# Kernel optimization log

Measured on AMD Instinct MI355X. Metric: run time of the kernel, lower is better.

The kernel has to match this reference:

```python
import jax, jax.numpy as jnp
import numpy as np

N_NODES = 100000
D_IN = 256
D_OUT = 128
N_EDGES = 1600000


def setup_inputs() -> dict:
    key = jax.random.key(0)
    k1, k2, k3, k4 = jax.random.split(key, 4)
    x = jax.random.normal(k1, (N_NODES, D_IN), dtype=jnp.float32)
    edge_index = jax.random.randint(k2, (2, N_EDGES), 0, N_NODES, dtype=jnp.int64)
    # GCNConv parameters (glorot-style scale)
    W = jax.random.normal(k3, (D_IN, D_OUT), dtype=jnp.float32) * (1.0 / np.sqrt(D_IN))
    b = jax.random.normal(k4, (D_OUT,), dtype=jnp.float32) * 0.01
    return {"x": x, "edge_index": edge_index, "W": W, "b": b}


def reference(x, edge_index, W, b):
    n = x.shape[0]
    # add self-loops (PyG GCNConv default)
    loop = jnp.arange(n, dtype=edge_index.dtype)
    src = jnp.concatenate([edge_index[0], loop])
    dst = jnp.concatenate([edge_index[1], loop])
    # symmetric normalization: deg^-1/2[src] * deg^-1/2[dst]
    ones = jnp.ones(src.shape[0], dtype=x.dtype)
    deg = jax.ops.segment_sum(ones, dst, num_segments=n)
    dinv = jnp.where(deg > 0, jax.lax.rsqrt(deg), 0.0)
    norm = dinv[src] * dinv[dst]  # [E+N]
    # linear transform at nodes, then gather-scale-scatter over edges
    h = x @ W  # [N, d_out]
    msg = h[src] * norm[:, None]  # [E+N, d_out]
    out = jax.ops.segment_sum(msg, dst, num_segments=n) + b
    # CRD.forward: relu then dropout (identity in eval mode)
    return jax.nn.relu(out)
```

## Files before the change

kernel.cpp:

```cpp
#include <hip/hip_runtime.h>
#include <stdint.h>

#define D_IN 256
#define D_OUT 128
#define MAXB 800
#define NCHUNK 256

typedef __attribute__((ext_vector_type(8))) short bf16x8;
typedef __attribute__((ext_vector_type(4))) float f32x4;

__device__ __forceinline__ unsigned short f2bf(float f) {
  union { float f; uint32_t u; } v; v.f = f;
  uint32_t u = v.u;
  uint32_t r = (u + 0x7FFFu + ((u >> 16) & 1u)) >> 16;
  return (unsigned short)r;
}
__device__ __forceinline__ float bf_lo(uint32_t u) {
  union { uint32_t u; float f; } v; v.u = u << 16; return v.f;
}
__device__ __forceinline__ float bf_hi(uint32_t u) {
  union { uint32_t u; float f; } v; v.u = u & 0xFFFF0000u; return v.f;
}

__global__ __launch_bounds__(256) void k_conv_w(const float* __restrict__ W,
                                                unsigned short* __restrict__ wt) {
  int idx = blockIdx.x * 256 + threadIdx.x;
  int n = idx >> 8;
  int k = idx & 255;
  wt[idx] = f2bf(W[k * D_OUT + n]);
}

__global__ __launch_bounds__(256) void k_gemm(const float* __restrict__ x,
                                              const unsigned short* __restrict__ wt,
                                              unsigned short* __restrict__ hp, int N) {
  int wave = threadIdx.x >> 6;
  int lane = threadIdx.x & 63;
  int m = lane & 15;
  int q = lane >> 4;
  int r0 = blockIdx.x * 64 + wave * 16;
  if (r0 >= N) return;

  bf16x8 a[8];
  const float* xrow = x + (size_t)(r0 + m) * D_IN + q * 8;
#pragma unroll
  for (int kt = 0; kt < 8; ++kt) {
    float4 u0 = *reinterpret_cast<const float4*>(xrow + kt * 32);
    float4 u1 = *reinterpret_cast<const float4*>(xrow + kt * 32 + 4);
    bf16x8 av;
    av[0] = (short)f2bf(u0.x); av[1] = (short)f2bf(u0.y);
    av[2] = (short)f2bf(u0.z); av[3] = (short)f2bf(u0.w);
    av[4] = (short)f2bf(u1.x); av[5] = (short)f2bf(u1.y);
    av[6] = (short)f2bf(u1.z); av[7] = (short)f2bf(u1.w);
    a[kt] = av;
  }

#pragma unroll
  for (int nt = 0; nt < 8; ++nt) {
    f32x4 acc = {0.f, 0.f, 0.f, 0.f};
    const unsigned short* wrow = wt + (size_t)(nt * 16 + m) * D_IN + q * 8;
#pragma unroll
    for (int kt = 0; kt < 8; ++kt) {
      bf16x8 bv = *reinterpret_cast<const bf16x8*>(wrow + kt * 32);
      acc = __builtin_amdgcn_mfma_f32_16x16x32_bf16(a[kt], bv, acc, 0, 0, 0);
    }
#pragma unroll
    for (int r = 0; r < 4; ++r) {
      int row = r0 + q * 4 + r;
      hp[(size_t)row * D_OUT + nt * 16 + m] = f2bf(acc[r]);
    }
  }
}

__global__ __launch_bounds__(256) void k_passA(const int* __restrict__ ei, int E, int CH,
                                               int NB, int* __restrict__ cntm) {
  __shared__ int bins[MAXB];
  int c = blockIdx.x;
  for (int b = threadIdx.x; b < NB; b += 256) bins[b] = 0;
  __syncthreads();
  int start = c * CH, end = min(E, start + CH);
  for (int eb = start + (int)threadIdx.x * 4; eb < end; eb += 1024) {
    int kmax = end - eb; if (kmax > 4) kmax = 4;
    if (kmax == 4) {
      int4 v = *reinterpret_cast<const int4*>(ei + E + eb);
      atomicAdd(&bins[v.x >> 7], 1);
      atomicAdd(&bins[v.y >> 7], 1);
      atomicAdd(&bins[v.z >> 7], 1);
      atomicAdd(&bins[v.w >> 7], 1);
    } else {
      for (int k = 0; k < kmax; ++k) atomicAdd(&bins[ei[E + eb + k] >> 7], 1);
    }
  }
  __syncthreads();
  for (int b = threadIdx.x; b < NB; b += 256) cntm[(size_t)b * NCHUNK + c] = bins[b];
}

__global__ __launch_bounds__(NCHUNK) void k_scanB1(const int* __restrict__ cntm,
                                                   int* __restrict__ ofs,
                                                   int* __restrict__ tot) {
  __shared__ int sc[NCHUNK];
  int b = blockIdx.x, t = threadIdx.x;
  int v = cntm[(size_t)b * NCHUNK + t];
  sc[t] = v;
  __syncthreads();
  for (int off = 1; off < NCHUNK; off <<= 1) {
    int val = (t >= off) ? sc[t - off] : 0;
    __syncthreads();
    sc[t] += val;
    __syncthreads();
  }
  ofs[(size_t)b * NCHUNK + t] = sc[t] - v;
  if (t == NCHUNK - 1) tot[b] = sc[t];
}

__global__ __launch_bounds__(256) void k_scanB2(const int* __restrict__ tot,
                                                int* __restrict__ base, int NB,
                                                int* __restrict__ nptr, int N, int E) {
  __shared__ int sc[256];
  int t = threadIdx.x;
  int v[4];
  int s = 0;
#pragma unroll
  for (int j = 0; j < 4; ++j) {
    int i = t * 4 + j;
    v[j] = (i < NB) ? tot[i] : 0;
    s += v[j];
  }
  sc[t] = s;
  __syncthreads();
  for (int off = 1; off < 256; off <<= 1) {
    int val = (t >= off) ? sc[t - off] : 0;
    __syncthreads();
    sc[t] += val;
    __syncthreads();
  }
  int ex = sc[t] - s;
#pragma unroll
  for (int j = 0; j < 4; ++j) {
    int i = t * 4 + j;
    if (i < NB) base[i] = ex;
    ex += v[j];
  }
  if (t == 0) nptr[N] = E;
}

__global__ __launch_bounds__(256) void k_passC(const int* __restrict__ ei, int E, int CH,
                                               int NB, const int* __restrict__ ofs,
                                               const int* __restrict__ base,
                                               int* __restrict__ P) {
  __shared__ int cur[MAXB];
  int c = blockIdx.x;
  for (int b = threadIdx.x; b < NB; b += 256)
    cur[b] = base[b] + ofs[(size_t)b * NCHUNK + c];
  __syncthreads();
  int start = c * CH, end = min(E, start + CH);
  for (int eb = start + (int)threadIdx.x * 4; eb < end; eb += 1024) {
    int kmax = end - eb; if (kmax > 4) kmax = 4;
    int s4[4], d4[4];
    if (kmax == 4) {
      int4 vs = *reinterpret_cast<const int4*>(ei + eb);
      int4 vd = *reinterpret_cast<const int4*>(ei + E + eb);
      s4[0] = vs.x; s4[1] = vs.y; s4[2] = vs.z; s4[3] = vs.w;
      d4[0] = vd.x; d4[1] = vd.y; d4[2] = vd.z; d4[3] = vd.w;
    } else {
      for (int k = 0; k < kmax; ++k) { s4[k] = ei[eb + k]; d4[k] = ei[E + eb + k]; }
    }
#pragma unroll
    for (int k = 0; k < 4; ++k) {
      if (k >= kmax) break;
      int d = d4[k];
      int p = atomicAdd(&cur[d >> 7], 1);
      P[p] = s4[k] | ((d & 127) << 17);
    }
  }
}

__global__ __launch_bounds__(256) void k_sortd(const int* __restrict__ P,
                                               const int* __restrict__ base,
                                               const int* __restrict__ tot,
                                               int* __restrict__ nptr,
                                               float* __restrict__ dinv,
                                               int* __restrict__ P2, int N) {
  __shared__ int ideg[128];
  __shared__ int sc[128];
  __shared__ int cur[128];
  int b = blockIdx.x, t = threadIdx.x;
  if (t < 128) ideg[t] = 0;
  __syncthreads();
  int s0 = base[b], T = tot[b];
  for (int i = s0 + t; i < s0 + T; i += 256) atomicAdd(&ideg[P[i] >> 17], 1);
  __syncthreads();
  if (t < 128) sc[t] = ideg[t];
  __syncthreads();
  for (int off = 1; off < 128; off <<= 1) {
    int v = (t < 128 && t >= off) ? sc[t - off] : 0;
    __syncthreads();
    if (t < 128) sc[t] += v;
    __syncthreads();
  }
  if (t < 128) {
    int exc = s0 + sc[t] - ideg[t];
    int node = b * 128 + t;
    if (node < N) {
      nptr[node] = exc;
      dinv[node] = rsqrtf(1.0f + (float)ideg[t]);
    }
    cur[t] = exc;
  }
  __syncthreads();
  for (int i = s0 + t; i < s0 + T; i += 256) {
    int pk = P[i];
    int p = atomicAdd(&cur[pk >> 17], 1);
    P2[p] = pk & 0x1FFFF;
  }
}

__global__ __launch_bounds__(256) void k_agg(const int* __restrict__ P2,
                                             const int* __restrict__ nptr,
                                             const uint4* __restrict__ hrows,
                                             const float* __restrict__ dinv,
                                             const float* __restrict__ bias,
                                             float* __restrict__ out, int N) {
  int wave = threadIdx.x >> 6, lane = threadIdx.x & 63;
  int node = blockIdx.x * 4 + wave;
  if (node >= N) return;
  int rs = nptr[node], re = nptr[node + 1];
  int j = lane >> 4, c = lane & 15;

  float acc[8];
#pragma unroll
  for (int k = 0; k < 8; ++k) acc[k] = 0.f;

  for (int e = rs + j; e < re; e += 4) {
    int src = P2[e];
    float r = dinv[src];
    uint4 u = hrows[(size_t)src * 16 + c];
    acc[0] += r * bf_lo(u.x); acc[1] += r * bf_hi(u.x);
    acc[2] += r * bf_lo(u.y); acc[3] += r * bf_hi(u.y);
    acc[4] += r * bf_lo(u.z); acc[5] += r * bf_hi(u.z);
    acc[6] += r * bf_lo(u.w); acc[7] += r * bf_hi(u.w);
  }
#pragma unroll
  for (int k = 0; k < 8; ++k) {
    acc[k] += __shfl_xor(acc[k], 16);
    acc[k] += __shfl_xor(acc[k], 32);
  }
  if (j == 0) {
    float rsn = dinv[node];
    uint4 uh = hrows[(size_t)node * 16 + c];
    float self[8] = {bf_lo(uh.x), bf_hi(uh.x), bf_lo(uh.y), bf_hi(uh.y),
                     bf_lo(uh.z), bf_hi(uh.z), bf_lo(uh.w), bf_hi(uh.w)};
    const float4* b4 = reinterpret_cast<const float4*>(bias);
    float4 b0 = b4[c * 2], b1 = b4[c * 2 + 1];
    float bb[8] = {b0.x, b0.y, b0.z, b0.w, b1.x, b1.y, b1.z, b1.w};
    float o[8];
#pragma unroll
    for (int k = 0; k < 8; ++k) {
      float v = rsn * (acc[k] + rsn * self[k]) + bb[k];
      o[k] = v > 0.f ? v : 0.f;
    }
    float4* orow = reinterpret_cast<float4*>(out + (size_t)node * D_OUT + c * 8);
    orow[0] = float4{o[0], o[1], o[2], o[3]};
    orow[1] = float4{o[4], o[5], o[6], o[7]};
  }
}

extern "C" void kernel_launch(void* const* d_in, const int* in_sizes, int n_in,
                              void* d_out, int out_size, void* d_ws, size_t ws_size,
                              hipStream_t stream) {
  const float* x = (const float*)d_in[0];
  const int* ei = (const int*)d_in[1];
  const float* W = (const float*)d_in[2];
  const float* bias = (const float*)d_in[3];
  int N = in_sizes[0] / D_IN;
  int E = in_sizes[1] / 2;
  float* out = (float*)d_out;

  int NB = (N + 127) >> 7;
  int CH = ((E + NCHUNK - 1) / NCHUNK + 3) & ~3;

  char* w = (char*)d_ws;
  size_t off = 0;
  auto alloc = [&](size_t bytes) -> void* {
    void* p = w + off;
    off = (off + bytes + 255) & ~(size_t)255;
    return p;
  };
  unsigned short* wt = (unsigned short*)alloc((size_t)D_IN * D_OUT * 2);
  unsigned short* hp = (unsigned short*)alloc((size_t)N * D_OUT * 2);
  float* dinv = (float*)alloc((size_t)N * 4);
  int* cntm = (int*)alloc((size_t)NB * NCHUNK * 4);
  int* ofs = (int*)alloc((size_t)NB * NCHUNK * 4);
  int* tot = (int*)alloc((size_t)NB * 4);
  int* base = (int*)alloc((size_t)NB * 4);
  int* nptr = (int*)alloc((size_t)(N + 1) * 4);
  int* P = (int*)alloc((size_t)E * 4);
  int* P2 = (int*)alloc((size_t)E * 4);
  (void)ws_size; (void)n_in; (void)out_size;

  k_conv_w<<<(D_IN * D_OUT) / 256, 256, 0, stream>>>(W, wt);
  k_gemm<<<(N + 63) / 64, 256, 0, stream>>>(x, wt, hp, N);
  k_passA<<<NCHUNK, 256, 0, stream>>>(ei, E, CH, NB, cntm);
  k_scanB1<<<NB, NCHUNK, 0, stream>>>(cntm, ofs, tot);
  k_scanB2<<<1, 256, 0, stream>>>(tot, base, NB, nptr, N, E);
  k_passC<<<NCHUNK, 256, 0, stream>>>(ei, E, CH, NB, ofs, base, P);
  k_sortd<<<NB, 256, 0, stream>>>(P, base, tot, nptr, dinv, P2, N);
  k_agg<<<(N + 3) / 4, 256, 0, stream>>>(P2, nptr, (const uint4*)hp, dinv, bias, out, N);
}
```

Measured before the change: 327.4 us.

## Co-schedule GEMM blocks with CSR build kernels and merge small launches

Merges the weight conversion into the histogram kernel and folds the second-level scan into the placement kernel, so each block recomputes the bin bases. The node GEMM is split across two grids, running alongside the placement and per-bin sort kernels so its dense work overlaps their atomic-bound phases. The GEMM loop is reordered to stream x with a one-step prefetch, keeping eight accumulators live instead of eight A fragments. The aggregation loop is unrolled by two for more loads in flight. Risks are redundant scan work in every placement block, higher register pressure, and a fixed 3:5 GEMM split that may not match the relative cost of the two stages.

```diff
diff --git a/kernel.cpp b/kernel.cpp
--- a/kernel.cpp
+++ b/kernel.cpp
@@ -22,59 +22,60 @@
   union { uint32_t u; float f; } v; v.u = u & 0xFFFF0000u; return v.f;
 }
 
-__global__ __launch_bounds__(256) void k_conv_w(const float* __restrict__ W,
-                                                unsigned short* __restrict__ wt) {
-  int idx = blockIdx.x * 256 + threadIdx.x;
-  int n = idx >> 8;
-  int k = idx & 255;
-  wt[idx] = f2bf(W[k * D_OUT + n]);
-}
-
-__global__ __launch_bounds__(256) void k_gemm(const float* __restrict__ x,
-                                              const unsigned short* __restrict__ wt,
-                                              unsigned short* __restrict__ hp, int N) {
-  int wave = threadIdx.x >> 6;
-  int lane = threadIdx.x & 63;
-  int m = lane & 15;
-  int q = lane >> 4;
-  int r0 = blockIdx.x * 64 + wave * 16;
+__device__ __forceinline__ void gemm_block(int bid, const float* __restrict__ x,
+                                           const unsigned short* __restrict__ wt,
+                                           unsigned short* __restrict__ hp, int N) {
+  int wave = threadIdx.x >> 6, lane = threadIdx.x & 63;
+  int m = lane & 15, q = lane >> 4;
+  int r0 = bid * 64 + wave * 16;
   if (r0 >= N) return;
-
-  bf16x8 a[8];
   const float* xrow = x + (size_t)(r0 + m) * D_IN + q * 8;
+
+  f32x4 acc[8];
+#pragma unroll
+  for (int nt = 0; nt < 8; ++nt) acc[nt] = f32x4{0.f, 0.f, 0.f, 0.f};
+
+  float4 u0 = *reinterpret_cast<const float4*>(xrow);
+  float4 u1 = *reinterpret_cast<const float4*>(xrow + 4);
 #pragma unroll
   for (int kt = 0; kt < 8; ++kt) {
-    float4 u0 = *reinterpret_cast<const float4*>(xrow + kt * 32);
-    float4 u1 = *reinterpret_cast<const float4*>(xrow + kt * 32 + 4);
-    bf16x8 av;
-    av[0] = (short)f2bf(u0.x); av[1] = (short)f2bf(u0.y);
-    av[2] = (short)f2bf(u0.z); av[3] = (short)f2bf(u0.w);
-    av[4] = (short)f2bf(u1.x); av[5] = (short)f2bf(u1.y);
-    av[6] = (short)f2bf(u1.z); av[7] = (short)f2bf(u1.w);
-    a[kt] = av;
-  }
-
-#pragma unroll
-  for (int nt = 0; nt < 8; ++nt) {
-    f32x4 acc = {0.f, 0.f, 0.f, 0.f};
-    const unsigned short* wrow = wt + (size_t)(nt * 16 + m) * D_IN + q * 8;
-#pragma unroll
-    for (int kt = 0; kt < 8; ++kt) {
-      bf16x8 bv = *reinterpret_cast<const bf16x8*>(wrow + kt * 32);
-      acc = __builtin_amdgcn_mfma_f32_16x16x32_bf16(a[kt], bv, acc, 0, 0, 0);
-    }
-#pragma unroll
-    for (int r = 0; r < 4; ++r) {
-      int row = r0 + q * 4 + r;
-      hp[(size_t)row * D_OUT + nt * 16 + m] = f2bf(acc[r]);
-    }
-  }
-}
-
-__global__ __launch_bounds__(256) void k_passA(const int* __restrict__ ei, int E, int CH,
-                                               int NB, int* __restrict__ cntm) {
+    float4 n0, n1;
+    if (kt < 7) {
+      n0 = *reinterpret_cast<const float4*>(xrow + (kt + 1) * 32);
+      n1 = *reinterpret_cast<const float4*>(xrow + (kt + 1) * 32 + 4);
+    }
+    bf16x8 a;
+    a[0] = (short)f2bf(u0.x); a[1] = (short)f2bf(u0.y);
+    a[2] = (short)f2bf(u0.z); a[3] = (short)f2bf(u0.w);
+    a[4] = (short)f2bf(u1.x); a[5] = (short)f2bf(u1.y);
+    a[6] = (short)f2bf(u1.z); a[7] = (short)f2bf(u1.w);
+    const unsigned short* wbase = wt + q * 8 + kt * 32;
+#pragma unroll
+    for (int nt = 0; nt < 8; ++nt) {
+      bf16x8 bv = *reinterpret_cast<const bf16x8*>(wbase + (size_t)(nt * 16 + m) * D_IN);
+      acc[nt] = __builtin_amdgcn_mfma_f32_16x16x32_bf16(a, bv, acc[nt], 0, 0, 0);
+    }
+    u0 = n0; u1 = n1;
+  }
+#pragma unroll
+  for (int nt = 0; nt < 8; ++nt)
+#pragma unroll
+    for (int r = 0; r < 4; ++r)
+      hp[(size_t)(r0 + q * 4 + r) * D_OUT + nt * 16 + m] = f2bf(acc[nt][r]);
+}
+
+__global__ __launch_bounds__(256) void k_prep(const float* __restrict__ W,
+                                              unsigned short* __restrict__ wt,
+                                              const int* __restrict__ ei, int E, int CH,
+                                              int NB, int* __restrict__ cntm) {
   __shared__ int bins[MAXB];
-  int c = blockIdx.x;
+  if (blockIdx.x < 128) {
+    int idx = blockIdx.x * 256 + threadIdx.x;
+    int n = idx >> 8, k = idx & 255;
+    wt[idx] = f2bf(W[k * D_OUT + n]);
+    return;
+  }
+  int c = blockIdx.x - 128;
   for (int b = threadIdx.x; b < NB; b += 256) bins[b] = 0;
   __syncthreads();
   int start = c * CH, end = min(E, start + CH);
@@ -94,9 +95,9 @@
   for (int b = threadIdx.x; b < NB; b += 256) cntm[(size_t)b * NCHUNK + c] = bins[b];
 }
 
-__global__ __launch_bounds__(NCHUNK) void k_scanB1(const int* __restrict__ cntm,
-                                                   int* __restrict__ ofs,
-                                                   int* __restrict__ tot) {
+__global__ __launch_bounds__(NCHUNK) void k_scan1(const int* __restrict__ cntm,
+                                                  int* __restrict__ ofs,
+                                                  int* __restrict__ tot) {
   __shared__ int sc[NCHUNK];
   int b = blockIdx.x, t = threadIdx.x;
   int v = cntm[(size_t)b * NCHUNK + t];
@@ -112,13 +113,20 @@
   if (t == NCHUNK - 1) tot[b] = sc[t];
 }
 
-__global__ __launch_bounds__(256) void k_scanB2(const int* __restrict__ tot,
-                                                int* __restrict__ base, int NB,
-                                                int* __restrict__ nptr, int N, int E) {
+__global__ __launch_bounds__(256, 4) void k_place_gemm(
+    const int* __restrict__ ei, int E, int CH, int NB,
+    const int* __restrict__ ofs, const int* __restrict__ tot,
+    int* __restrict__ basep, int* __restrict__ P,
+    const float* __restrict__ x, const unsigned short* __restrict__ wt,
+    unsigned short* __restrict__ hp, int N) {
   __shared__ int sc[256];
-  int t = threadIdx.x;
-  int v[4];
-  int s = 0;
+  __shared__ int cur[MAXB];
+  if (blockIdx.x >= NCHUNK) {
+    gemm_block(blockIdx.x - NCHUNK, x, wt, hp, N);
+    return;
+  }
+  int c = blockIdx.x, t = threadIdx.x;
+  int v[4]; int s = 0;
 #pragma unroll
   for (int j = 0; j < 4; ++j) {
     int i = t * 4 + j;
@@ -137,23 +145,15 @@
 #pragma unroll
   for (int j = 0; j < 4; ++j) {
     int i = t * 4 + j;
-    if (i < NB) base[i] = ex;
+    if (i < NB) cur[i] = ex + ofs[(size_t)i * NCHUNK + c];
     ex += v[j];
   }
-  if (t == 0) nptr[N] = E;
-}
-
-__global__ __launch_bounds__(256) void k_passC(const int* __restrict__ ei, int E, int CH,
-                                               int NB, const int* __restrict__ ofs,
-                                               const int* __restrict__ base,
-                                               int* __restrict__ P) {
-  __shared__ int cur[MAXB];
-  int c = blockIdx.x;
-  for (int b = threadIdx.x; b < NB; b += 256)
-    cur[b] = base[b] + ofs[(size_t)b * NCHUNK + c];
-  __syncthreads();
+  __syncthreads();
+  if (c == 0) {
+    for (int b = t; b < NB; b += 256) basep[b] = cur[b];
+  }
   int start = c * CH, end = min(E, start + CH);
-  for (int eb = start + (int)threadIdx.x * 4; eb < end; eb += 1024) {
+  for (int eb = start + t * 4; eb < end; eb += 1024) {
     int kmax = end - eb; if (kmax > 4) kmax = 4;
     int s4[4], d4[4];
     if (kmax == 4) {
@@ -174,19 +174,24 @@
   }
 }
 
-__global__ __launch_bounds__(256) void k_sortd(const int* __restrict__ P,
-                                               const int* __restrict__ base,
-                                               const int* __restrict__ tot,
-                                               int* __restrict__ nptr,
-                                               float* __restrict__ dinv,
-                                               int* __restrict__ P2, int N) {
+__global__ __launch_bounds__(256, 4) void k_sort_gemm(
+    const int* __restrict__ P, const int* __restrict__ basep,
+    const int* __restrict__ tot, int* __restrict__ nptr, float* __restrict__ dinv,
+    int* __restrict__ P2, int N, int E, int NB,
+    const float* __restrict__ x, const unsigned short* __restrict__ wt,
+    unsigned short* __restrict__ hp, int Goff) {
   __shared__ int ideg[128];
   __shared__ int sc[128];
   __shared__ int cur[128];
+  if (blockIdx.x >= (unsigned)NB) {
+    gemm_block(blockIdx.x - NB + Goff, x, wt, hp, N);
+    return;
+  }
   int b = blockIdx.x, t = threadIdx.x;
+  if (b == 0 && t == 0) nptr[N] = E;
   if (t < 128) ideg[t] = 0;
   __syncthreads();
-  int s0 = base[b], T = tot[b];
+  int s0 = basep[b], T = tot[b];
   for (int i = s0 + t; i < s0 + T; i += 256) atomicAdd(&ideg[P[i] >> 17], 1);
   __syncthreads();
   if (t < 128) sc[t] = ideg[t];
@@ -230,14 +235,29 @@
 #pragma unroll
   for (int k = 0; k < 8; ++k) acc[k] = 0.f;
 
-  for (int e = rs + j; e < re; e += 4) {
-    int src = P2[e];
-    float r = dinv[src];
-    uint4 u = hrows[(size_t)src * 16 + c];
-    acc[0] += r * bf_lo(u.x); acc[1] += r * bf_hi(u.x);
-    acc[2] += r * bf_lo(u.y); acc[3] += r * bf_hi(u.y);
-    acc[4] += r * bf_lo(u.z); acc[5] += r * bf_hi(u.z);
-    acc[6] += r * bf_lo(u.w); acc[7] += r * bf_hi(u.w);
+  int e = rs + j;
+  for (; e + 4 < re; e += 8) {
+    int sA = P2[e], sB = P2[e + 4];
+    float rA = dinv[sA], rB = dinv[sB];
+    uint4 uA = hrows[(size_t)sA * 16 + c];
+    uint4 uB = hrows[(size_t)sB * 16 + c];
+    acc[0] += rA * bf_lo(uA.x) + rB * bf_lo(uB.x);
+    acc[1] += rA * bf_hi(uA.x) + rB * bf_hi(uB.x);
+    acc[2] += rA * bf_lo(uA.y) + rB * bf_lo(uB.y);
+    acc[3] += rA * bf_hi(uA.y) + rB * bf_hi(uB.y);
+    acc[4] += rA * bf_lo(uA.z) + rB * bf_lo(uB.z);
+    acc[5] += rA * bf_hi(uA.z) + rB * bf_hi(uB.z);
+    acc[6] += rA * bf_lo(uA.w) + rB * bf_lo(uB.w);
+    acc[7] += rA * bf_hi(uA.w) + rB * bf_hi(uB.w);
+  }
+  if (e < re) {
+    int sA = P2[e];
+    float rA = dinv[sA];
+    uint4 uA = hrows[(size_t)sA * 16 + c];
+    acc[0] += rA * bf_lo(uA.x); acc[1] += rA * bf_hi(uA.x);
+    acc[2] += rA * bf_lo(uA.y); acc[3] += rA * bf_hi(uA.y);
+    acc[4] += rA * bf_lo(uA.z); acc[5] += rA * bf_hi(uA.z);
+    acc[6] += rA * bf_lo(uA.w); acc[7] += rA * bf_hi(uA.w);
   }
 #pragma unroll
   for (int k = 0; k < 8; ++k) {
@@ -291,18 +311,21 @@
   int* cntm = (int*)alloc((size_t)NB * NCHUNK * 4);
   int* ofs = (int*)alloc((size_t)NB * NCHUNK * 4);
   int* tot = (int*)alloc((size_t)NB * 4);
-  int* base = (int*)alloc((size_t)NB * 4);
+  int* basep = (int*)alloc((size_t)NB * 4);
   int* nptr = (int*)alloc((size_t)(N + 1) * 4);
   int* P = (int*)alloc((size_t)E * 4);
   int* P2 = (int*)alloc((size_t)E * 4);
   (void)ws_size; (void)n_in; (void)out_size;
 
-  k_conv_w<<<(D_IN * D_OUT) / 256, 256, 0, stream>>>(W, wt);
-  k_gemm<<<(N + 63) / 64, 256, 0, stream>>>(x, wt, hp, N);
-  k_passA<<<NCHUNK, 256, 0, stream>>>(ei, E, CH, NB, cntm);
-  k_scanB1<<<NB, NCHUNK, 0, stream>>>(cntm, ofs, tot);
-  k_scanB2<<<1, 256, 0, stream>>>(tot, base, NB, nptr, N, E);
-  k_passC<<<NCHUNK, 256, 0, stream>>>(ei, E, CH, NB, ofs, base, P);
-  k_sortd<<<NB, 256, 0, stream>>>(P, base, tot, nptr, dinv, P2, N);
+  int Gg = (N + 63) / 64;
+  int Gg1 = (Gg * 3) / 5;
+  int Gg2 = Gg - Gg1;
+
+  k_prep<<<128 + NCHUNK, 256, 0, stream>>>(W, wt, ei, E, CH, NB, cntm);
+  k_scan1<<<NB, NCHUNK, 0, stream>>>(cntm, ofs, tot);
+  k_place_gemm<<<NCHUNK + Gg1, 256, 0, stream>>>(ei, E, CH, NB, ofs, tot, basep, P,
+                                                 x, wt, hp, N);
+  k_sort_gemm<<<NB + Gg2, 256, 0, stream>>>(P, basep, tot, nptr, dinv, P2, N, E, NB,
+                                            x, wt, hp, Gg1);
   k_agg<<<(N + 3) / 4, 256, 0, stream>>>(P2, nptr, (const uint4*)hp, dinv, bias, out, N);
 }
```

Measured after the change: 332.0 us. About the same (+1.4%).
